# Kernel optimization log

Measured on AMD Instinct MI355X. Metric: run time of the kernel, lower is better.

Reference implementation:

```python
import jax, jax.numpy as jnp
import numpy as np

B, T, NH, HD = 2, 2048, 12, 128
HIDDEN = NH * HD
EPS = 1.1920928955078125e-07  # torch fp32 finfo eps (F.rms_norm default)


def _rope_cos_sin(T, d_half, base=10000.0):
    inv = 1.0 / (base ** (jnp.arange(d_half, dtype=jnp.float32) / d_half))
    t = jnp.arange(T, dtype=jnp.float32)
    f = t[:, None] * inv[None, :]  # [T, d_half]
    return jnp.cos(f)[None, :, None, :], jnp.sin(f)[None, :, None, :]


def apply_rotary_emb(x, cos, sin):
    d = x.shape[3] // 2
    x1, x2 = x[..., :d], x[..., d:]
    return jnp.concatenate([x1 * cos + x2 * sin, x1 * -sin + x2 * cos], axis=3)


def rms_norm(x):
    return x * jax.lax.rsqrt(jnp.mean(x * x, axis=-1, keepdims=True) + EPS)


def setup_inputs() -> dict:
    key = jax.random.key(0)
    ks = jax.random.split(key, 5)
    x = jax.random.normal(ks[0], (B, T, HIDDEN), dtype=jnp.float32)
    cos, sin = _rope_cos_sin(T, HD // 2)
    s = 1.0 / np.sqrt(HIDDEN)
    Wq = jax.random.normal(ks[1], (HIDDEN, HIDDEN), dtype=jnp.float32) * s
    Wk = jax.random.normal(ks[2], (HIDDEN, HIDDEN), dtype=jnp.float32) * s
    Wv = jax.random.normal(ks[3], (HIDDEN, HIDDEN), dtype=jnp.float32) * s
    Wp = jax.random.normal(ks[4], (HIDDEN, HIDDEN), dtype=jnp.float32) * s
    return {"x": x, "cos": cos, "sin": sin, "Wq": Wq, "Wk": Wk, "Wv": Wv,
            "Wp": Wp, "window": 1024}


def reference(x, cos, sin, Wq, Wk, Wv, Wp, window):
    Bx, Tx, _ = x.shape
    q = (x @ Wq.T).reshape(Bx, Tx, NH, HD)
    k = (x @ Wk.T).reshape(Bx, Tx, NH, HD)
    v = (x @ Wv.T).reshape(Bx, Tx, NH, HD)
    q = rms_norm(apply_rotary_emb(q, cos, sin))
    k = rms_norm(apply_rotary_emb(k, cos, sin))
    # causal + sliding-window attention (dense, matching the sdpa fallback)
    scale = 1.0 / np.sqrt(HD)
    scores = jnp.einsum('bqhd,bkhd->bhqk', q, k) * scale
    row = jnp.arange(Tx)[:, None]
    col = jnp.arange(Tx)[None, :]
    mask = (col <= row) & (row - col <= window)
    scores = jnp.where(mask[None, None], scores, jnp.finfo(scores.dtype).min)
    attn = jax.nn.softmax(scores, axis=-1)
    y = jnp.einsum('bhqk,bkhd->bqhd', attn, v).reshape(Bx, Tx, HIDDEN)
    return y @ Wp.T
```

## Files before the change

### kernel.cpp

```cpp
#include <hip/hip_runtime.h>
#include <stdint.h>

#define HIDDEN 1536
#define NHEAD 12
#define HD 128
#define TSEQ 2048
#define NROWS 4096
#define KDIM HIDDEN
#define EPS_F 1.1920928955078125e-07f
#define SCALE_LOG2E 0.12751879110195655f
#define FIXSUB 16.6f

typedef unsigned short u16;
typedef __bf16 bf16x8_t __attribute__((ext_vector_type(8)));
typedef float f32x4_t __attribute__((ext_vector_type(4)));

#define MFMA16(a, b, c) __builtin_amdgcn_mfma_f32_16x16x32_bf16((a), (b), (c), 0, 0, 0)
#define GLL(srcp, dstp) \
  __builtin_amdgcn_global_load_lds((const __attribute__((address_space(1))) void*)(srcp), \
                                   (__attribute__((address_space(3))) void*)(dstp), 16, 0, 0)

__device__ __forceinline__ u16 f2bf(float f) {
  unsigned u = __builtin_bit_cast(unsigned, f);
  u = (u + 0x7fffu + ((u >> 16) & 1u)) >> 16;
  return (u16)u;
}
__device__ __forceinline__ float bfu(u16 v) {
  return __builtin_bit_cast(float, ((unsigned)v) << 16);
}

__global__ __launch_bounds__(256) void cast_kernel(const float* __restrict__ in,
                                                   u16* __restrict__ out, int n) {
  int i = (blockIdx.x * 256 + threadIdx.x) * 4;
  if (i >= n) return;
  float4 v = *reinterpret_cast<const float4*>(in + i);
  uint2 pk;
  pk.x = (unsigned)f2bf(v.x) | ((unsigned)f2bf(v.y) << 16);
  pk.y = (unsigned)f2bf(v.z) | ((unsigned)f2bf(v.w) << 16);
  *reinterpret_cast<uint2*>(out + i) = pk;
}

__global__ __launch_bounds__(256) void cast4_kernel(
    const float* __restrict__ a, const float* __restrict__ b, const float* __restrict__ c,
    const float* __restrict__ d, u16* __restrict__ oa, u16* __restrict__ ob,
    u16* __restrict__ oc, u16* __restrict__ od, int n) {
  const float* in;
  u16* out;
  switch (blockIdx.y) {
    case 0: in = a; out = oa; break;
    case 1: in = b; out = ob; break;
    case 2: in = c; out = oc; break;
    default: in = d; out = od; break;
  }
  int i = (blockIdx.x * 256 + threadIdx.x) * 4;
  if (i >= n) return;
  float4 v = *reinterpret_cast<const float4*>(in + i);
  uint2 pk;
  pk.x = (unsigned)f2bf(v.x) | ((unsigned)f2bf(v.y) << 16);
  pk.y = (unsigned)f2bf(v.z) | ((unsigned)f2bf(v.w) << 16);
  *reinterpret_cast<uint2*>(out + i) = pk;
}

__global__ __launch_bounds__(512, 2) void gemm_qkv_kernel(
    const u16* __restrict__ xb, const u16* __restrict__ wq, const u16* __restrict__ wk,
    const u16* __restrict__ wv, const float* __restrict__ cosp, const float* __restrict__ sinp,
    u16* __restrict__ qh, u16* __restrict__ kh, u16* __restrict__ vt) {
  __shared__ __align__(16) u16 lds[49152];
  const int tid = threadIdx.x;
  const int bid = blockIdx.x;
  const int xcd = bid & 7, cc = bid >> 3;
  const int m = xcd * 2 + (cc & 1);
  const int nz = cc >> 1;
  const int z = nz / 12, n = nz % 12;
  const int M0 = m * 256, N0 = n * 128;
  const u16* W = (z == 0) ? wq : (z == 1) ? wk : wv;
  const int w = tid >> 6, l = tid & 63;
  const int lrow = l & 15, kg = l >> 4;
  const int wm = w >> 1, wn = w & 1;
  const int srow = tid >> 3;
  const unsigned jsw = (unsigned)(((tid & 7) ^ (srow & 7)) * 8);
  const u16* pA0 = xb + (size_t)(M0 + srow) * KDIM + jsw;
  const u16* pA1 = xb + (size_t)(M0 + 128 + srow) * KDIM + jsw;
  const u16* pB = W + (size_t)(N0 + srow) * KDIM + jsw;
  const size_t R64 = (size_t)64 * KDIM;
  u16* dst0 = lds + w * 512;
  auto stage = [&](const u16* p, int buf, int i) {
    u16* db = dst0 + buf * 24576 + i * 8192;
    GLL(p, db);
    GLL(p + R64, db + 4096);
  };
  stage(pA0, 0, 0);
  stage(pA1, 0, 1);
  stage(pB, 0, 2);
  pA0 += 64; pA1 += 64; pB += 64;
  asm volatile("s_waitcnt vmcnt(0)" ::: "memory");
  __builtin_amdgcn_s_barrier();
  asm volatile("" ::: "memory");
  f32x4_t acc[4][4] = {};
  const int aoff = (wm >> 1) * 8192;
  const int arow0 = (wm & 1) * 64;
  const int swz = lrow & 7;
  const int NT = KDIM / 64;
#pragma unroll 1
  for (int T = 0; T < NT; ++T) {
    const int buf = T & 1;
    const u16* Ab = lds + buf * 24576 + aoff;
    const u16* Bb = lds + buf * 24576 + 16384;
    bf16x8_t bfr[4][2], afr[2][2];
#pragma unroll
    for (int nf = 0; nf < 4; ++nf)
#pragma unroll
      for (int ks = 0; ks < 2; ++ks)
        bfr[nf][ks] = *reinterpret_cast<const bf16x8_t*>(
            Bb + (wn * 64 + nf * 16 + lrow) * 64 + (((ks << 2) | kg) ^ swz) * 8);
#pragma unroll
    for (int mf = 0; mf < 2; ++mf)
#pragma unroll
      for (int ks = 0; ks < 2; ++ks)
        afr[mf][ks] = *reinterpret_cast<const bf16x8_t*>(
            Ab + (arow0 + mf * 16 + lrow) * 64 + (((ks << 2) | kg) ^ swz) * 8);
    if (T + 1 < NT) {
      stage(pA0, buf ^ 1, 0);
      stage(pA1, buf ^ 1, 1);
    }
    __builtin_amdgcn_s_barrier();
    asm volatile("" ::: "memory");
    __builtin_amdgcn_s_setprio(1);
#pragma unroll
    for (int mf = 0; mf < 2; ++mf)
#pragma unroll
      for (int nf = 0; nf < 4; ++nf)
#pragma unroll
        for (int ks = 0; ks < 2; ++ks)
          acc[mf][nf] = MFMA16(afr[mf][ks], bfr[nf][ks], acc[mf][nf]);
    __builtin_amdgcn_s_setprio(0);
    __builtin_amdgcn_s_barrier();
    asm volatile("" ::: "memory");
    bf16x8_t afr2[2][2];
#pragma unroll
    for (int mf = 0; mf < 2; ++mf)
#pragma unroll
      for (int ks = 0; ks < 2; ++ks)
        afr2[mf][ks] = *reinterpret_cast<const bf16x8_t*>(
            Ab + (arow0 + (mf + 2) * 16 + lrow) * 64 + (((ks << 2) | kg) ^ swz) * 8);
    if (T + 1 < NT) {
      stage(pB, buf ^ 1, 2);
      pA0 += 64; pA1 += 64; pB += 64;
    }
    __builtin_amdgcn_s_barrier();
    asm volatile("" ::: "memory");
    __builtin_amdgcn_s_setprio(1);
#pragma unroll
    for (int mf = 0; mf < 2; ++mf)
#pragma unroll
      for (int nf = 0; nf < 4; ++nf)
#pragma unroll
        for (int ks = 0; ks < 2; ++ks)
          acc[mf + 2][nf] = MFMA16(afr2[mf][ks], bfr[nf][ks], acc[mf + 2][nf]);
    __builtin_amdgcn_s_setprio(0);
    asm volatile("s_waitcnt vmcnt(0)" ::: "memory");
    __builtin_amdgcn_s_barrier();
    asm volatile("" ::: "memory");
  }
  char* cs = reinterpret_cast<char*>(lds);
  const int bb = M0 >> 11;
  const int t0 = M0 & (TSEQ - 1);
  const size_t bhn = (size_t)(bb * NHEAD + n);
  if (z == 2) {
#pragma unroll
    for (int mf = 0; mf < 4; ++mf)
#pragma unroll
      for (int nf = 0; nf < 4; ++nf)
#pragma unroll
        for (int r = 0; r < 4; ++r) {
          const int trow = wm * 64 + mf * 16 + kg * 4 + r;
          const int d = wn * 64 + nf * 16 + lrow;
          const int bofs = (d * 512 + trow * 2) ^ ((d & 7) << 4);
          *reinterpret_cast<u16*>(cs + bofs) = f2bf(acc[mf][nf][r]);
        }
    __syncthreads();
    const int d = tid >> 2, tq = tid & 3;
    u16* dst = vt + (bhn * HD + d) * TSEQ + t0 + tq * 64;
    const char* rb = cs + d * 512 + tq * 128;
#pragma unroll
    for (int j = 0; j < 8; ++j) {
      uint4 v = *reinterpret_cast<const uint4*>(rb + ((j ^ (d & 7)) * 16));
      *reinterpret_cast<uint4*>(dst + j * 8) = v;
    }
  } else {
#pragma unroll
    for (int mf = 0; mf < 4; ++mf)
#pragma unroll
      for (int nf = 0; nf < 4; ++nf)
#pragma unroll
        for (int r = 0; r < 4; ++r) {
          const int trow = wm * 64 + mf * 16 + kg * 4 + r;
          const int d = wn * 64 + nf * 16 + lrow;
          const int bofs = (trow * 256 + d * 2) ^ ((trow & 7) << 4);
          *reinterpret_cast<u16*>(cs + bofs) = f2bf(acc[mf][nf][r]);
        }
    __syncthreads();
    const int rr = tid >> 1, hh = tid & 1;
    const int t = t0 + rr;
    const float* cosb = cosp + t * 64;
    const float* sinb = sinp + t * 64;
    const char* base = cs + rr * 256;
    float ss = 0.0f;
    unsigned pk[32];
#pragma unroll
    for (int j = 0; j < 8; ++j) {
      const int jp = (j ^ (rr & 7)) * 16;
      uint4 vo = *reinterpret_cast<const uint4*>(base + hh * 128 + jp);
      uint4 vx = *reinterpret_cast<const uint4*>(base + (hh ^ 1) * 128 + jp);
      const unsigned vo32[4] = {vo.x, vo.y, vo.z, vo.w};
      const unsigned vx32[4] = {vx.x, vx.y, vx.z, vx.w};
      const float* cj = cosb + j * 8;
      const float* sj = sinb + j * 8;
#pragma unroll
      for (int q2 = 0; q2 < 4; ++q2) {
        float o0 = bfu((u16)(vo32[q2] & 0xffffu)), o1 = bfu((u16)(vo32[q2] >> 16));
        float x0 = bfu((u16)(vx32[q2] & 0xffffu)), x1 = bfu((u16)(vx32[q2] >> 16));
        float cc0 = cj[q2 * 2], cc1 = cj[q2 * 2 + 1];
        float s0 = sj[q2 * 2], s1 = sj[q2 * 2 + 1];
        float y0 = hh ? __builtin_fmaf(o0, cc0, -x0 * s0) : __builtin_fmaf(o0, cc0, x0 * s0);
        float y1 = hh ? __builtin_fmaf(o1, cc1, -x1 * s1) : __builtin_fmaf(o1, cc1, x1 * s1);
        ss = __builtin_fmaf(y0, y0, __builtin_fmaf(y1, y1, ss));
        pk[j * 4 + q2] = (unsigned)f2bf(y0) | ((unsigned)f2bf(y1) << 16);
      }
    }
    ss += __shfl_xor(ss, 1, 64);
    const float rinv = rsqrtf(ss * (1.0f / 128.0f) + EPS_F);
    u16* dst = ((z == 0) ? qh : kh) + (bhn * TSEQ + t) * HD + hh * 64;
#pragma unroll
    for (int j = 0; j < 8; ++j) {
      unsigned o[4];
#pragma unroll
      for (int q2 = 0; q2 < 4; ++q2) {
        float y0 = bfu((u16)(pk[j * 4 + q2] & 0xffffu)) * rinv;
        float y1 = bfu((u16)(pk[j * 4 + q2] >> 16)) * rinv;
        o[q2] = (unsigned)f2bf(y0) | ((unsigned)f2bf(y1) << 16);
      }
      uint4 v;
      v.x = o[0]; v.y = o[1]; v.z = o[2]; v.w = o[3];
      *reinterpret_cast<uint4*>(dst + j * 8) = v;
    }
  }
}

__device__ __forceinline__ void gemm_mainloop64(const u16* __restrict__ A,
                                                const u16* __restrict__ W, int M0, int N0,
                                                u16* lds, f32x4_t acc[4][4], int tid) {
  const int w = tid >> 6, l = tid & 63;
  const int lrow = l & 15, kg = l >> 4;
  const int wr = (w >> 1) * 64, wc = (w & 1) * 64;
  const int row0 = tid >> 3, j0 = tid & 7;
  const unsigned jsw = (unsigned)((j0 ^ (row0 & 7)) * 8);
  unsigned offA = (unsigned)((M0 + row0) * KDIM) + jsw;
  unsigned offW = (unsigned)((N0 + row0) * KDIM) + jsw;
  const u16* A1 = A + 32 * KDIM; const u16* A2 = A + 64 * KDIM; const u16* A3 = A + 96 * KDIM;
  const u16* W1 = W + 32 * KDIM; const u16* W2 = W + 64 * KDIM; const u16* W3 = W + 96 * KDIM;
  auto issue = [&](int buf) {
    u16* da = lds + buf * 8192 + w * 512;
    u16* dw = lds + 16384 + buf * 8192 + w * 512;
    GLL(A + offA, da);          GLL(A1 + offA, da + 2048);
    GLL(A2 + offA, da + 4096);  GLL(A3 + offA, da + 6144);
    GLL(W + offW, dw);          GLL(W1 + offW, dw + 2048);
    GLL(W2 + offW, dw + 4096);  GLL(W3 + offW, dw + 6144);
    offA += 64; offW += 64;
  };
  issue(0);
  const int NT = KDIM / 64;
#pragma unroll 1
  for (int kt = 0; kt < NT; ++kt) {
    const int cur = kt & 1;
    if (kt + 1 < NT) {
      issue(cur ^ 1);
      asm volatile("s_waitcnt vmcnt(8)" ::: "memory");
    } else {
      asm volatile("s_waitcnt vmcnt(0)" ::: "memory");
    }
    __builtin_amdgcn_s_barrier();
    asm volatile("" ::: "memory");
    const u16* Ab = lds + cur * 8192;
    const u16* Wb = lds + 16384 + cur * 8192;
#pragma unroll
    for (int s = 0; s < 2; ++s) {
      bf16x8_t af[4], bf_[4];
#pragma unroll
      for (int mi = 0; mi < 4; ++mi) {
        const int row = wr + mi * 16 + lrow;
        af[mi] = *reinterpret_cast<const bf16x8_t*>(Ab + row * 64 +
                                                    (((s << 2) | kg) ^ (row & 7)) * 8);
      }
#pragma unroll
      for (int ni = 0; ni < 4; ++ni) {
        const int row = wc + ni * 16 + lrow;
        bf_[ni] = *reinterpret_cast<const bf16x8_t*>(Wb + row * 64 +
                                                     (((s << 2) | kg) ^ (row & 7)) * 8);
      }
#pragma unroll
      for (int mi = 0; mi < 4; ++mi)
#pragma unroll
        for (int ni = 0; ni < 4; ++ni)
          acc[mi][ni] = MFMA16(af[mi], bf_[ni], acc[mi][ni]);
    }
    asm volatile("s_waitcnt lgkmcnt(0)" ::: "memory");
    __builtin_amdgcn_s_barrier();
    asm volatile("" ::: "memory");
  }
}

__global__ __launch_bounds__(256) void gemm_out_kernel(const u16* __restrict__ yh,
                                                       const u16* __restrict__ wp,
                                                       float* __restrict__ out) {
  __shared__ __align__(16) u16 lds[32768];
  const int tid = threadIdx.x;
  const int wgid = blockIdx.x;
  const int xcd = wgid & 7, c = wgid >> 3;
  const int m = ((xcd & 3) << 3) + (c & 7);
  const int n = ((xcd >> 2) * 6) + (c >> 3);
  const int M0 = m * 128, N0 = n * 128;
  f32x4_t acc[4][4] = {};
  gemm_mainloop64(yh, wp, M0, N0, lds, acc, tid);
  const int w = tid >> 6, l = tid & 63;
  const int lrow = l & 15, kg = l >> 4;
  const int wr = (w >> 1) * 64, wc = (w & 1) * 64;
#pragma unroll
  for (int mi = 0; mi < 4; ++mi)
#pragma unroll
    for (int ni = 0; ni < 4; ++ni)
#pragma unroll
      for (int r = 0; r < 4; ++r) {
        const int grow = M0 + wr + mi * 16 + kg * 4 + r;
        const int gcol = N0 + wc + ni * 16 + lrow;
        out[(size_t)grow * HIDDEN + gcol] = acc[mi][ni][r];
      }
}

__global__ __launch_bounds__(512, 4) void attn_kernel(const u16* __restrict__ qh,
                                                      const u16* __restrict__ kh,
                                                      const u16* __restrict__ vt,
                                                      u16* __restrict__ yh,
                                                      const int* __restrict__ winp) {
  __shared__ __align__(16) u16 Kl[2][8192];
  __shared__ __align__(16) u16 Vl[2][8192];
  __shared__ __align__(16) u16 Pl[8][1024];
  const int tid = threadIdx.x, w = tid >> 6, l = tid & 63;
  const int lrow = l & 15, kg = l >> 4;
  const int bid = blockIdx.x;
  const int swz = (bid & 7) * 48 + (bid >> 3);
  const int qb = swz & 15;
  const int bh = swz >> 4;
  const int h = bh % NHEAD, b = bh / NHEAD;
  const int win = winp[0];
  const u16* Q = qh + (size_t)bh * TSEQ * HD;
  const u16* K = kh + (size_t)bh * TSEQ * HD;
  const u16* V = vt + (size_t)bh * HD * TSEQ;
  const int qw = qb * 128 + w * 16;
  bf16x8_t aq[4];
#pragma unroll
  for (int ks = 0; ks < 4; ++ks)
    aq[ks] = *reinterpret_cast<const bf16x8_t*>(Q + (qw + lrow) * HD + ks * 32 + kg * 8);
  float lsum[4] = {0.f, 0.f, 0.f, 0.f};
  f32x4_t accv[8] = {};
  int lo = qb * 128 - win;
  if (lo < 0) lo = 0;
  lo &= ~63;
  const int last = qb * 128 + 64;

  u16* Pw = &Pl[w][0];

  auto stage_k = [&](int kv, int buf) {
#pragma unroll
    for (int i = 0; i < 2; ++i) {
      const int c = i * 512 + w * 64 + l;
      const int row = c >> 4, j = c & 15;
      const u16* src = K + (size_t)(kv + row) * HD + ((j ^ (row & 7)) * 8);
      GLL(src, &Kl[buf][0] + i * 4096 + w * 512);
    }
  };
  auto stage_v = [&](int kv, int buf) {
#pragma unroll
    for (int i = 0; i < 2; ++i) {
      const int c = i * 512 + w * 64 + l;
      const int row = c >> 3, j = c & 7;
      const u16* src = V + (size_t)row * TSEQ + kv + ((j ^ (row & 7)) * 8);
      GLL(src, &Vl[buf][0] + i * 4096 + w * 512);
    }
  };

  stage_k(lo, 0);
  stage_v(lo, 0);
  int it = 0;
  for (int kv = lo; kv <= last; kv += 64, ++it) {
    const int cur = it & 1;
    const int kpre = (kv + 64 <= last) ? kv + 64 : last;
    stage_k(kpre, cur ^ 1);
    asm volatile("s_waitcnt vmcnt(2)" ::: "memory");
    __builtin_amdgcn_s_barrier();
    asm volatile("" ::: "memory");
    stage_v(kpre, cur ^ 1);
    const u16* Kb = &Kl[cur][0];
    f32x4_t s[4] = {};
#pragma unroll
    for (int n = 0; n < 4; ++n) {
      const int row = n * 16 + lrow;
#pragma unroll
      for (int ks = 0; ks < 4; ++ks) {
        bf16x8_t bk = *reinterpret_cast<const bf16x8_t*>(
            Kb + row * 128 + (((ks << 2) | kg) ^ (row & 7)) * 8);
        s[n] = MFMA16(aq[ks], bk, s[n]);
      }
    }
    float ps[4][4];
    const bool interior = (kv + 63 <= qw) && ((qw + 15) - kv <= win);
    if (interior) {
#pragma unroll
      for (int n = 0; n < 4; ++n)
#pragma unroll
        for (int r = 0; r < 4; ++r)
          ps[n][r] = exp2f(__builtin_fmaf(s[n][r], SCALE_LOG2E, -FIXSUB));
    } else {
#pragma unroll
      for (int n = 0; n < 4; ++n) {
        const int key = kv + n * 16 + lrow;
#pragma unroll
        for (int r = 0; r < 4; ++r) {
          const int rowq = qw + kg * 4 + r;
          const bool ok = (key <= rowq) && (rowq - key <= win);
          ps[n][r] = ok ? exp2f(__builtin_fmaf(s[n][r], SCALE_LOG2E, -FIXSUB)) : 0.0f;
        }
      }
    }
#pragma unroll
    for (int r = 0; r < 4; ++r)
      lsum[r] += (ps[0][r] + ps[1][r]) + (ps[2][r] + ps[3][r]);
#pragma unroll
    for (int n = 0; n < 4; ++n)
#pragma unroll
      for (int r = 0; r < 4; ++r) {
        const int rp = kg * 4 + r;
        int bofs = rp * 128 + (n * 16 + lrow) * 2;
        bofs ^= (rp & 7) << 4;
        *reinterpret_cast<u16*>(reinterpret_cast<char*>(Pw) + bofs) = f2bf(ps[n][r]);
      }
    asm volatile("s_waitcnt lgkmcnt(0)" ::: "memory");
    __builtin_amdgcn_s_barrier();
    asm volatile("" ::: "memory");
    bf16x8_t ap[2];
#pragma unroll
    for (int k2 = 0; k2 < 2; ++k2) {
      int bofs = lrow * 128 + k2 * 64 + kg * 16;
      bofs ^= (lrow & 7) << 4;
      ap[k2] = *reinterpret_cast<const bf16x8_t*>(reinterpret_cast<const char*>(Pw) + bofs);
    }
    const u16* Vb = &Vl[cur][0];
#pragma unroll
    for (int k2 = 0; k2 < 2; ++k2)
#pragma unroll
      for (int dn = 0; dn < 8; ++dn) {
        const int row = dn * 16 + lrow;
        bf16x8_t bv = *reinterpret_cast<const bf16x8_t*>(
            Vb + row * 64 + (((k2 << 2) | kg) ^ (row & 7)) * 8);
        accv[dn] = MFMA16(ap[k2], bv, accv[dn]);
      }
  }
#pragma unroll
  for (int off = 1; off < 16; off <<= 1)
#pragma unroll
    for (int r = 0; r < 4; ++r) lsum[r] += __shfl_xor(lsum[r], off, 64);
  float inv[4];
#pragma unroll
  for (int r = 0; r < 4; ++r) inv[r] = 1.0f / lsum[r];
#pragma unroll
  for (int dn = 0; dn < 8; ++dn)
#pragma unroll
    for (int r = 0; r < 4; ++r) {
      const int rowg = b * TSEQ + qw + kg * 4 + r;
      const int col = h * HD + dn * 16 + lrow;
      yh[(size_t)rowg * HIDDEN + col] = f2bf(accv[dn][r] * inv[r]);
    }
}

extern "C" void kernel_launch(void* const* d_in, const int* in_sizes, int n_in, void* d_out,
                              int out_size, void* d_ws, size_t ws_size, hipStream_t stream) {
  const float* x = (const float*)d_in[0];
  const float* cosp = (const float*)d_in[1];
  const float* sinp = (const float*)d_in[2];
  const float* Wq = (const float*)d_in[3];
  const float* Wk = (const float*)d_in[4];
  const float* Wv = (const float*)d_in[5];
  const float* Wp = (const float*)d_in[6];
  const int* winp = (const int*)d_in[7];

  char* ws = (char*)d_ws;
  size_t off = 0;
  auto alloc = [&](size_t bytes) {
    char* p = ws + off;
    off += (bytes + 255) & ~(size_t)255;
    return p;
  };
  u16* xb = (u16*)alloc((size_t)NROWS * HIDDEN * 2);
  u16* wqb = (u16*)alloc((size_t)HIDDEN * HIDDEN * 2);
  u16* wkb = (u16*)alloc((size_t)HIDDEN * HIDDEN * 2);
  u16* wvb = (u16*)alloc((size_t)HIDDEN * HIDDEN * 2);
  u16* wpb = (u16*)alloc((size_t)HIDDEN * HIDDEN * 2);
  u16* qh = (u16*)alloc((size_t)NROWS * HIDDEN * 2);
  u16* kh = (u16*)alloc((size_t)NROWS * HIDDEN * 2);
  u16* vt = (u16*)alloc((size_t)NROWS * HIDDEN * 2);
  u16* yh = (u16*)alloc((size_t)NROWS * HIDDEN * 2);

  const int nx = NROWS * HIDDEN;
  const int nw = HIDDEN * HIDDEN;
  cast_kernel<<<nx / 1024, 256, 0, stream>>>(x, xb, nx);
  cast4_kernel<<<dim3(nw / 1024, 4), 256, 0, stream>>>(Wq, Wk, Wv, Wp, wqb, wkb, wvb, wpb, nw);

  gemm_qkv_kernel<<<dim3(576), 512, 0, stream>>>(xb, wqb, wkb, wvb, cosp, sinp, qh, kh, vt);
  attn_kernel<<<dim3(384), 512, 0, stream>>>(qh, kh, vt, yh, winp);
  gemm_out_kernel<<<dim3(384), 256, 0, stream>>>(yh, wpb, (float*)d_out);
}
```

Before: 203.8 us.

## Restructure QKV GEMM main loop into simpler double-buffered prefetch schedule

Replaces the two-phase main loop of the QKV projection GEMM, which split A staging across MFMA halves with four barriers per K-step and setprio hints. The new loop issues all six global-to-LDS loads for the next tile up front, waits with vmcnt(6) so only the current tile must be resident, and then does two k-substeps, each loading 4 A and 4 B fragments before 16 MFMAs. It uses 32-bit offsets instead of pointers and needs only two barriers per iteration. The intent is to cut barrier and scheduling overhead and let loads overlap a whole iteration of compute. The cost is that it drops the setprio hints and the finer interleaving of loads with MFMAs.

```diff
diff --git a/kernel.cpp b/kernel.cpp
--- a/kernel.cpp
+++ b/kernel.cpp
@@ -79,86 +79,59 @@
   const int wm = w >> 1, wn = w & 1;
   const int srow = tid >> 3;
   const unsigned jsw = (unsigned)(((tid & 7) ^ (srow & 7)) * 8);
-  const u16* pA0 = xb + (size_t)(M0 + srow) * KDIM + jsw;
-  const u16* pA1 = xb + (size_t)(M0 + 128 + srow) * KDIM + jsw;
-  const u16* pB = W + (size_t)(N0 + srow) * KDIM + jsw;
+  unsigned offA = (unsigned)((M0 + srow) * KDIM) + jsw;
+  unsigned offB = (unsigned)((N0 + srow) * KDIM) + jsw;
   const size_t R64 = (size_t)64 * KDIM;
-  u16* dst0 = lds + w * 512;
-  auto stage = [&](const u16* p, int buf, int i) {
-    u16* db = dst0 + buf * 24576 + i * 8192;
-    GLL(p, db);
-    GLL(p + R64, db + 4096);
+  auto issue = [&](int buf) {
+    u16* da = lds + buf * 24576 + w * 512;
+    u16* db = lds + buf * 24576 + 16384 + w * 512;
+    GLL(xb + offA, da);
+    GLL(xb + offA + R64, da + 4096);
+    GLL(xb + offA + 2 * R64, da + 8192);
+    GLL(xb + offA + 3 * R64, da + 12288);
+    GLL(W + offB, db);
+    GLL(W + offB + R64, db + 4096);
+    offA += 64;
+    offB += 64;
   };
-  stage(pA0, 0, 0);
-  stage(pA1, 0, 1);
-  stage(pB, 0, 2);
-  pA0 += 64; pA1 += 64; pB += 64;
-  asm volatile("s_waitcnt vmcnt(0)" ::: "memory");
-  __builtin_amdgcn_s_barrier();
-  asm volatile("" ::: "memory");
+  issue(0);
   f32x4_t acc[4][4] = {};
-  const int aoff = (wm >> 1) * 8192;
-  const int arow0 = (wm & 1) * 64;
-  const int swz = lrow & 7;
   const int NT = KDIM / 64;
 #pragma unroll 1
-  for (int T = 0; T < NT; ++T) {
-    const int buf = T & 1;
-    const u16* Ab = lds + buf * 24576 + aoff;
-    const u16* Bb = lds + buf * 24576 + 16384;
-    bf16x8_t bfr[4][2], afr[2][2];
-#pragma unroll
-    for (int nf = 0; nf < 4; ++nf)
-#pragma unroll
-      for (int ks = 0; ks < 2; ++ks)
-        bfr[nf][ks] = *reinterpret_cast<const bf16x8_t*>(
-            Bb + (wn * 64 + nf * 16 + lrow) * 64 + (((ks << 2) | kg) ^ swz) * 8);
-#pragma unroll
-    for (int mf = 0; mf < 2; ++mf)
-#pragma unroll
-      for (int ks = 0; ks < 2; ++ks)
-        afr[mf][ks] = *reinterpret_cast<const bf16x8_t*>(
-            Ab + (arow0 + mf * 16 + lrow) * 64 + (((ks << 2) | kg) ^ swz) * 8);
-    if (T + 1 < NT) {
-      stage(pA0, buf ^ 1, 0);
-      stage(pA1, buf ^ 1, 1);
-    }
-    __builtin_amdgcn_s_barrier();
-    asm volatile("" ::: "memory");
-    __builtin_amdgcn_s_setprio(1);
-#pragma unroll
-    for (int mf = 0; mf < 2; ++mf)
-#pragma unroll
-      for (int nf = 0; nf < 4; ++nf)
-#pragma unroll
-        for (int ks = 0; ks < 2; ++ks)
-          acc[mf][nf] = MFMA16(afr[mf][ks], bfr[nf][ks], acc[mf][nf]);
-    __builtin_amdgcn_s_setprio(0);
-    __builtin_amdgcn_s_barrier();
-    asm volatile("" ::: "memory");
-    bf16x8_t afr2[2][2];
-#pragma unroll
-    for (int mf = 0; mf < 2; ++mf)
-#pragma unroll
-      for (int ks = 0; ks < 2; ++ks)
-        afr2[mf][ks] = *reinterpret_cast<const bf16x8_t*>(
-            Ab + (arow0 + (mf + 2) * 16 + lrow) * 64 + (((ks << 2) | kg) ^ swz) * 8);
-    if (T + 1 < NT) {
-      stage(pB, buf ^ 1, 2);
-      pA0 += 64; pA1 += 64; pB += 64;
-    }
-    __builtin_amdgcn_s_barrier();
-    asm volatile("" ::: "memory");
-    __builtin_amdgcn_s_setprio(1);
-#pragma unroll
-    for (int mf = 0; mf < 2; ++mf)
-#pragma unroll
-      for (int nf = 0; nf < 4; ++nf)
-#pragma unroll
-        for (int ks = 0; ks < 2; ++ks)
-          acc[mf + 2][nf] = MFMA16(afr2[mf][ks], bfr[nf][ks], acc[mf + 2][nf]);
-    __builtin_amdgcn_s_setprio(0);
-    asm volatile("s_waitcnt vmcnt(0)" ::: "memory");
+  for (int kt = 0; kt < NT; ++kt) {
+    const int cur = kt & 1;
+    if (kt + 1 < NT) {
+      issue(cur ^ 1);
+      asm volatile("s_waitcnt vmcnt(6)" ::: "memory");
+    } else {
+      asm volatile("s_waitcnt vmcnt(0)" ::: "memory");
+    }
+    __builtin_amdgcn_s_barrier();
+    asm volatile("" ::: "memory");
+    const u16* Ab = lds + cur * 24576;
+    const u16* Bb = Ab + 16384;
+#pragma unroll
+    for (int s = 0; s < 2; ++s) {
+      bf16x8_t af[4], bf_[4];
+#pragma unroll
+      for (int mi = 0; mi < 4; ++mi) {
+        const int row = wm * 64 + mi * 16 + lrow;
+        af[mi] = *reinterpret_cast<const bf16x8_t*>(Ab + row * 64 +
+                                                    (((s << 2) | kg) ^ (row & 7)) * 8);
+      }
+#pragma unroll
+      for (int ni = 0; ni < 4; ++ni) {
+        const int row = wn * 64 + ni * 16 + lrow;
+        bf_[ni] = *reinterpret_cast<const bf16x8_t*>(Bb + row * 64 +
+                                                     (((s << 2) | kg) ^ (row & 7)) * 8);
+      }
+#pragma unroll
+      for (int mi = 0; mi < 4; ++mi)
+#pragma unroll
+        for (int ni = 0; ni < 4; ++ni)
+          acc[mi][ni] = MFMA16(af[mi], bf_[ni], acc[mi][ni]);
+    }
+    asm volatile("s_waitcnt lgkmcnt(0)" ::: "memory");
     __builtin_amdgcn_s_barrier();
     asm volatile("" ::: "memory");
   }
```

Measured after the change: 198.7 us. -2.5%, faster.
